# Kernel tuning notes

Measured on AMD Instinct MI355X. Metric: run time of the kernel, lower is better.

The kernel has to match this reference:

```python
import jax, jax.numpy as jnp
import numpy as np

EPS = 1e-8
ALPHA = 0.3
PATTERN_W = 0.1


def setup_inputs() -> dict:
    key = jax.random.key(0)
    ks = jax.random.split(key, 6)
    H, W, D, Hid = 1024, 1024, 32, 64
    return {
        "grid_states": jax.random.normal(ks[0], (H, W, D), dtype=jnp.float32),
        "potentials": jax.random.uniform(ks[1], (H, W), dtype=jnp.float32),
        "W1": jax.random.normal(ks[2], (D + 1, Hid), dtype=jnp.float32) * 0.1,
        "b1": jax.random.normal(ks[3], (Hid,), dtype=jnp.float32) * 0.1,
        "W2": jax.random.normal(ks[4], (Hid, D), dtype=jnp.float32) * 0.1,
        "b2": jax.random.normal(ks[5], (D,), dtype=jnp.float32) * 0.1,
    }


def reference(grid_states, potentials, W1, b1, W2, b2):
    # self_similarity: A^3 normalized to unit length, rescaled by ||A||
    cube = grid_states * grid_states * grid_states                     # [H,W,D]
    cube_norm = jnp.linalg.norm(cube, axis=-1, keepdims=True)          # [H,W,1]
    cell_norm = jnp.linalg.norm(grid_states, axis=-1, keepdims=True)   # [H,W,1]
    self_pattern = cube / (cube_norm + EPS) * cell_norm                # [H,W,D]

    cell_with_pattern = grid_states + PATTERN_W * self_pattern         # [H,W,D]

    # transform_net on [cell_with_pattern ; potential]
    x = jnp.concatenate([cell_with_pattern, potentials[..., None]], axis=-1)  # [H,W,D+1]
    h = jax.nn.relu(jnp.einsum("hwc,cf->hwf", x, W1) + b1)             # [H,W,Hid]
    transformed = jnp.einsum("hwf,fd->hwd", h, W2) + b2                # [H,W,D]

    # new_state = transform + alpha * cell  (neighbor influence path only
    # affects role_value, which forward() discards)
    return transformed + ALPHA * grid_states
```

## Files before the change

### kernel.cpp

```cpp
#include <hip/hip_runtime.h>

#define DIM   32
#define HID   64
#define TILES 8

typedef __attribute__((ext_vector_type(8))) short bf16x8;
typedef __attribute__((ext_vector_type(4))) float f32x4;

__device__ __forceinline__ unsigned cvt_pk_bf16(float lo, float hi) {
    unsigned r;
    asm("v_cvt_pk_bf16_f32 %0, %1, %2" : "=v"(r) : "v"(lo), "v"(hi));
    return r;
}

__device__ __forceinline__ void plswap(unsigned &a, unsigned &b) {
    auto r = __builtin_amdgcn_permlane32_swap((int)a, (int)b, false, false);
    a = (unsigned)r[0];
    b = (unsigned)r[1];
}

struct f2 { float a, b; };
__device__ __forceinline__ f2 plswap16v(float a, float b) {
    auto r = __builtin_amdgcn_permlane16_swap(__float_as_int(a), __float_as_int(b),
                                              false, false);
    return { __int_as_float(r[0]), __int_as_float(r[1]) };
}

__device__ __forceinline__ float quad_sum(float x) {
    auto r1 = __builtin_amdgcn_permlane32_swap(__float_as_int(x), __float_as_int(x),
                                               false, false);
    float t = __int_as_float(r1[0]) + __int_as_float(r1[1]);
    auto r2 = __builtin_amdgcn_permlane16_swap(__float_as_int(t), __float_as_int(t),
                                               false, false);
    return __int_as_float(r2[0]) + __int_as_float(r2[1]);
}

union bfu { bf16x8 v; unsigned u[4]; };

__global__ __launch_bounds__(256, 3) void behavior_mfma(
    const float* __restrict__ g_in,
    const float* __restrict__ pot,
    const float* __restrict__ W1,
    const float* __restrict__ b1,
    const float* __restrict__ W2,
    const float* __restrict__ b2,
    float* __restrict__ out)
{
    const int tid  = threadIdx.x;
    const int lane = tid & 63;
    const int quad = lane >> 4;
    const int mrow = lane & 15;
    const int wave = tid >> 6;

    const long cell0 = ((long)blockIdx.x * 4 + wave) * (TILES * 16);

    float4 gA[2], gB[2]; float pV[2];
    auto loadT = [&](int s, long cb) {
        const float* gp = g_in + (cb + mrow) * DIM + quad * 8;
        gA[s] = ((const float4*)gp)[0];
        gB[s] = ((const float4*)gp)[1];
        pV[s] = pot[cb + mrow];
    };
    loadT(0, cell0);
    loadT(1, cell0 + 16);

    bf16x8 w1f[4];
    #pragma unroll
    for (int nb = 0; nb < 4; ++nb) {
        bfu t;
        #pragma unroll
        for (int jp = 0; jp < 4; ++jp)
            t.u[jp] = cvt_pk_bf16(W1[(quad * 8 + 2 * jp)     * HID + nb * 16 + mrow],
                                  W1[(quad * 8 + 2 * jp + 1) * HID + nb * 16 + mrow]);
        w1f[nb] = t.v;
    }
    bf16x8 w2f[2][2];
    #pragma unroll
    for (int kc = 0; kc < 2; ++kc)
        #pragma unroll
        for (int nc = 0; nc < 2; ++nc) {
            bfu t;
            #pragma unroll
            for (int jp = 0; jp < 4; ++jp) {
                const int j0 = 2 * jp;
                const int r0 = kc * 32 + (quad >> 1) * 16 + (quad & 1) * 4
                             + ((j0 >> 2) << 3) + (j0 & 3);
                t.u[jp] = cvt_pk_bf16(W2[r0 * DIM + nc * 16 + mrow],
                                      W2[(r0 + 1) * DIM + nc * 16 + mrow]);
            }
            w2f[kc][nc] = t.v;
        }
    bf16x8 aid[2];
    #pragma unroll
    for (int nc = 0; nc < 2; ++nc) {
        bfu t;
        #pragma unroll
        for (int jp = 0; jp < 4; ++jp) {
            unsigned lo = (quad * 8 + 2 * jp     == nc * 16 + mrow) ? 0x00003F80u : 0u;
            unsigned hi = (quad * 8 + 2 * jp + 1 == nc * 16 + mrow) ? 0x3F800000u : 0u;
            t.u[jp] = lo | hi;
        }
        aid[nc] = t.v;
    }
    float w1pq[4][4], b1q[4][4];
    #pragma unroll
    for (int nb = 0; nb < 4; ++nb)
        #pragma unroll
        for (int r = 0; r < 4; ++r) {
            w1pq[nb][r] = W1[32 * HID + nb * 16 + quad * 4 + r];
            b1q[nb][r]  = b1[nb * 16 + quad * 4 + r];
        }
    float b2q[2][4];
    #pragma unroll
    for (int nc = 0; nc < 2; ++nc)
        #pragma unroll
        for (int r = 0; r < 4; ++r)
            b2q[nc][r] = b2[nc * 16 + quad * 4 + r];

    auto stageA = [&](int s, bfu& h0, bfu& h1, bfu& gf) {
        const float4 a = gA[s], b = gB[s];
        const float potv = pV[s];

        float gv[8] = {a.x, a.y, a.z, a.w, b.x, b.y, b.z, b.w};
        float cube[8];
        float tp = 0.f, sp = 0.f;
        #pragma unroll
        for (int j = 0; j < 8; ++j) {
            float gc = gv[j];
            float g2 = gc * gc;
            float g3 = g2 * gc;
            tp += g2;
            sp = fmaf(g3, g3, sp);
            cube[j] = g3;
        }
        tp = quad_sum(tp);
        sp = quad_sum(sp);
        const float scale = 0.1f * __builtin_amdgcn_sqrtf(tp) *
                            __builtin_amdgcn_rcpf(__builtin_amdgcn_sqrtf(sp) + 1e-8f);

        bfu xf;
        #pragma unroll
        for (int jp = 0; jp < 4; ++jp) {
            xf.u[jp] = cvt_pk_bf16(fmaf(scale, cube[2 * jp],     gv[2 * jp]),
                                   fmaf(scale, cube[2 * jp + 1], gv[2 * jp + 1]));
            gf.u[jp] = cvt_pk_bf16(0.3f * gv[2 * jp], 0.3f * gv[2 * jp + 1]);
        }

        unsigned P[4][2];
        #pragma unroll
        for (int nb = 0; nb < 4; ++nb) {
            f32x4 c1;
            #pragma unroll
            for (int r = 0; r < 4; ++r)
                c1[r] = fmaf(potv, w1pq[nb][r], b1q[nb][r]);
            c1 = __builtin_amdgcn_mfma_f32_16x16x32_bf16(w1f[nb], xf.v, c1, 0, 0, 0);
            P[nb][0] = cvt_pk_bf16(fmaxf(c1[0], 0.f), fmaxf(c1[1], 0.f));
            P[nb][1] = cvt_pk_bf16(fmaxf(c1[2], 0.f), fmaxf(c1[3], 0.f));
        }

        {
            unsigned x0 = P[0][0], y0 = P[1][0]; plswap(x0, y0);
            unsigned x1 = P[0][1], y1 = P[1][1]; plswap(x1, y1);
            h0.u[0] = x0; h0.u[1] = x1; h0.u[2] = y0; h0.u[3] = y1;
        }
        {
            unsigned x0 = P[2][0], y0 = P[3][0]; plswap(x0, y0);
            unsigned x1 = P[2][1], y1 = P[3][1]; plswap(x1, y1);
            h1.u[0] = x0; h1.u[1] = x1; h1.u[2] = y0; h1.u[3] = y1;
        }
    };

    auto gemm2st = [&](const bfu& h0, const bfu& h1, const bfu& gf, long cb) {
        f32x4 A, B;
        #pragma unroll
        for (int nc = 0; nc < 2; ++nc) {
            f32x4 c2 = {b2q[nc][0], b2q[nc][1], b2q[nc][2], b2q[nc][3]};
            c2 = __builtin_amdgcn_mfma_f32_16x16x32_bf16(aid[nc],    gf.v, c2, 0, 0, 0);
            c2 = __builtin_amdgcn_mfma_f32_16x16x32_bf16(w2f[0][nc], h0.v, c2, 0, 0, 0);
            c2 = __builtin_amdgcn_mfma_f32_16x16x32_bf16(w2f[1][nc], h1.v, c2, 0, 0, 0);
            if (nc == 0) A = c2; else B = c2;
        }
        #pragma unroll
        for (int r = 0; r < 4; ++r) {
            float ar = A[r], br = B[r];
            f2 sw = plswap16v(ar, br);
            A[r] = sw.a; B[r] = sw.b;
        }
        const int colq = ((quad & 1) << 4) | ((quad >> 1) << 3);
        float* op = out + (cb + mrow) * DIM + colq;
        *(f32x4*)op       = A;
        *(f32x4*)(op + 4) = B;
    };

    bfu h0P, h1P, gfP;
    stageA(0, h0P, h1P, gfP);
    loadT(0, cell0 + 32);

    #pragma unroll
    for (int t = 1; t < TILES; ++t) {
        const int s = t & 1;
        bfu h0C, h1C, gfC;
        stageA(s, h0C, h1C, gfC);
        if (t + 2 < TILES) loadT(s, cell0 + (long)(t + 2) * 16);
        gemm2st(h0P, h1P, gfP, cell0 + (long)(t - 1) * 16);
        h0P = h0C; h1P = h1C; gfP = gfC;
    }
    gemm2st(h0P, h1P, gfP, cell0 + (long)(TILES - 1) * 16);
}

extern "C" void kernel_launch(void* const* d_in, const int* in_sizes, int n_in,
                              void* d_out, int out_size, void* d_ws, size_t ws_size,
                              hipStream_t stream) {
    const float* g_in = (const float*)d_in[0];
    const float* pot  = (const float*)d_in[1];
    const float* W1   = (const float*)d_in[2];
    const float* b1   = (const float*)d_in[3];
    const float* W2   = (const float*)d_in[4];
    const float* b2   = (const float*)d_in[5];
    float* out = (float*)d_out;

    const int n_cells = in_sizes[1];
    const int cells_per_block = 4 * TILES * 16;
    const int blocks = (n_cells + cells_per_block - 1) / cells_per_block;

    behavior_mfma<<<blocks, 256, 0, stream>>>(g_in, pot, W1, b1, W2, b2, out);
}
```

Baseline: 245.5 us.

## Deepen input prefetch to three tiles, shrink blocks, pack bias constants as bf16

Increases the software prefetch depth from two to three 16-cell tiles per wave so more global loads are in flight while the MFMA stages run. Blocks shrink from 256 to 128 threads (2 waves), doubling the grid. To offset the extra prefetch registers, the W1 potential row, b1 and b2 are stored packed as bf16 pairs and unpacked on use. This lowers bias precision slightly and adds a few ALU ops per tile, and the extra buffer may raise register pressure and reduce occupancy.

```diff
diff --git a/kernel.cpp b/kernel.cpp
--- a/kernel.cpp
+++ b/kernel.cpp
@@ -12,6 +12,8 @@
     asm("v_cvt_pk_bf16_f32 %0, %1, %2" : "=v"(r) : "v"(lo), "v"(hi));
     return r;
 }
+__device__ __forceinline__ float bfp_lo(unsigned u) { return __uint_as_float(u << 16); }
+__device__ __forceinline__ float bfp_hi(unsigned u) { return __uint_as_float(u & 0xFFFF0000u); }
 
 __device__ __forceinline__ void plswap(unsigned &a, unsigned &b) {
     auto r = __builtin_amdgcn_permlane32_swap((int)a, (int)b, false, false);
@@ -37,7 +39,7 @@
 
 union bfu { bf16x8 v; unsigned u[4]; };
 
-__global__ __launch_bounds__(256, 3) void behavior_mfma(
+__global__ __launch_bounds__(128, 3) void behavior_mfma(
     const float* __restrict__ g_in,
     const float* __restrict__ pot,
     const float* __restrict__ W1,
@@ -52,9 +54,9 @@
     const int mrow = lane & 15;
     const int wave = tid >> 6;
 
-    const long cell0 = ((long)blockIdx.x * 4 + wave) * (TILES * 16);
-
-    float4 gA[2], gB[2]; float pV[2];
+    const long cell0 = ((long)blockIdx.x * 2 + wave) * (TILES * 16);
+
+    float4 gA[3], gB[3]; float pV[3];
     auto loadT = [&](int s, long cb) {
         const float* gp = g_in + (cb + mrow) * DIM + quad * 8;
         gA[s] = ((const float4*)gp)[0];
@@ -63,6 +65,7 @@
     };
     loadT(0, cell0);
     loadT(1, cell0 + 16);
+    loadT(2, cell0 + 32);
 
     bf16x8 w1f[4];
     #pragma unroll
@@ -102,20 +105,23 @@
         }
         aid[nc] = t.v;
     }
-    float w1pq[4][4], b1q[4][4];
+    unsigned w1pp[4][2], b1p[4][2];
     #pragma unroll
     for (int nb = 0; nb < 4; ++nb)
         #pragma unroll
-        for (int r = 0; r < 4; ++r) {
-            w1pq[nb][r] = W1[32 * HID + nb * 16 + quad * 4 + r];
-            b1q[nb][r]  = b1[nb * 16 + quad * 4 + r];
-        }
-    float b2q[2][4];
+        for (int p = 0; p < 2; ++p) {
+            w1pp[nb][p] = cvt_pk_bf16(W1[32 * HID + nb * 16 + quad * 4 + 2 * p],
+                                      W1[32 * HID + nb * 16 + quad * 4 + 2 * p + 1]);
+            b1p[nb][p]  = cvt_pk_bf16(b1[nb * 16 + quad * 4 + 2 * p],
+                                      b1[nb * 16 + quad * 4 + 2 * p + 1]);
+        }
+    unsigned b2p[2][2];
     #pragma unroll
     for (int nc = 0; nc < 2; ++nc)
         #pragma unroll
-        for (int r = 0; r < 4; ++r)
-            b2q[nc][r] = b2[nc * 16 + quad * 4 + r];
+        for (int p = 0; p < 2; ++p)
+            b2p[nc][p] = cvt_pk_bf16(b2[nc * 16 + quad * 4 + 2 * p],
+                                     b2[nc * 16 + quad * 4 + 2 * p + 1]);
 
     auto stageA = [&](int s, bfu& h0, bfu& h1, bfu& gf) {
         const float4 a = gA[s], b = gB[s];
@@ -150,9 +156,10 @@
         #pragma unroll
         for (int nb = 0; nb < 4; ++nb) {
             f32x4 c1;
-            #pragma unroll
-            for (int r = 0; r < 4; ++r)
-                c1[r] = fmaf(potv, w1pq[nb][r], b1q[nb][r]);
+            c1[0] = fmaf(potv, bfp_lo(w1pp[nb][0]), bfp_lo(b1p[nb][0]));
+            c1[1] = fmaf(potv, bfp_hi(w1pp[nb][0]), bfp_hi(b1p[nb][0]));
+            c1[2] = fmaf(potv, bfp_lo(w1pp[nb][1]), bfp_lo(b1p[nb][1]));
+            c1[3] = fmaf(potv, bfp_hi(w1pp[nb][1]), bfp_hi(b1p[nb][1]));
             c1 = __builtin_amdgcn_mfma_f32_16x16x32_bf16(w1f[nb], xf.v, c1, 0, 0, 0);
             P[nb][0] = cvt_pk_bf16(fmaxf(c1[0], 0.f), fmaxf(c1[1], 0.f));
             P[nb][1] = cvt_pk_bf16(fmaxf(c1[2], 0.f), fmaxf(c1[3], 0.f));
@@ -174,7 +181,11 @@
         f32x4 A, B;
         #pragma unroll
         for (int nc = 0; nc < 2; ++nc) {
-            f32x4 c2 = {b2q[nc][0], b2q[nc][1], b2q[nc][2], b2q[nc][3]};
+            f32x4 c2;
+            c2[0] = bfp_lo(b2p[nc][0]);
+            c2[1] = bfp_hi(b2p[nc][0]);
+            c2[2] = bfp_lo(b2p[nc][1]);
+            c2[3] = bfp_hi(b2p[nc][1]);
             c2 = __builtin_amdgcn_mfma_f32_16x16x32_bf16(aid[nc],    gf.v, c2, 0, 0, 0);
             c2 = __builtin_amdgcn_mfma_f32_16x16x32_bf16(w2f[0][nc], h0.v, c2, 0, 0, 0);
             c2 = __builtin_amdgcn_mfma_f32_16x16x32_bf16(w2f[1][nc], h1.v, c2, 0, 0, 0);
@@ -194,14 +205,14 @@
 
     bfu h0P, h1P, gfP;
     stageA(0, h0P, h1P, gfP);
-    loadT(0, cell0 + 32);
+    loadT(0, cell0 + (long)3 * 16);
 
     #pragma unroll
     for (int t = 1; t < TILES; ++t) {
-        const int s = t & 1;
+        const int s = t % 3;
         bfu h0C, h1C, gfC;
         stageA(s, h0C, h1C, gfC);
-        if (t + 2 < TILES) loadT(s, cell0 + (long)(t + 2) * 16);
+        if (t + 3 < TILES) loadT(s, cell0 + (long)(t + 3) * 16);
         gemm2st(h0P, h1P, gfP, cell0 + (long)(t - 1) * 16);
         h0P = h0C; h1P = h1C; gfP = gfC;
     }
@@ -220,8 +231,8 @@
     float* out = (float*)d_out;
 
     const int n_cells = in_sizes[1];
-    const int cells_per_block = 4 * TILES * 16;
+    const int cells_per_block = 2 * TILES * 16;
     const int blocks = (n_cells + cells_per_block - 1) / cells_per_block;
 
-    behavior_mfma<<<blocks, 256, 0, stream>>>(g_in, pot, W1, b1, W2, b2, out);
-}
+    behavior_mfma<<<blocks, 128, 0, stream>>>(g_in, pot, W1, b1, W2, b2, out);
+}
```

Result: no change. 247.8 us (+1.0%).
